# Kernel tuning notes

Hardware: AMD Instinct MI355X
Metric: run time of the kernel (lower is better)

The kernel has to match this reference:

```python
import jax, jax.numpy as jnp
import numpy as np

N, E, H = 50000, 500000, 4
DIN, DH, DO, TD = 135, 128, 64, 9

def _ln(x, g, b):
    mu = jnp.mean(x, axis=-1, keepdims=True)
    v = jnp.var(x, axis=-1, keepdims=True)
    return (x - mu) / jnp.sqrt(v + 1e-5) * g + b

def _gat(x, src, dst, W, a_src, a_dst, b, n, heads, c):
    h = (x @ W).reshape(n, heads, c)                      # [N,H,C]
    es = jnp.sum(h * a_src, -1)                           # [N,H]
    ed = jnp.sum(h * a_dst, -1)
    e = jax.nn.leaky_relu(es[src] + ed[dst], 0.2)         # [E,H]
    m = jax.ops.segment_max(e, dst, num_segments=n)       # segment softmax over dst
    ex = jnp.exp(e - m[dst])
    den = jax.ops.segment_sum(ex, dst, num_segments=n)
    alpha = ex / (den[dst] + 1e-16)
    out = jax.ops.segment_sum(h[src] * alpha[..., None], dst, num_segments=n)
    return jnp.mean(out, axis=1) + b                      # concat=False -> head mean

def setup_inputs() -> dict:
    key = jax.random.key(0)
    ks = jax.random.split(key, 32)
    rn = lambda i, shape: jax.random.normal(ks[i], shape, jnp.float32) * 0.05
    inp = {}
    inp['x'] = jax.random.normal(ks[0], (N, DIN), jnp.float32)
    inp['edge_index'] = jax.random.randint(ks[1], (2, E), 0, N, jnp.int32)
    inp['edge_attr'] = jnp.ones((E, 1), jnp.float32)
    inp['W_in'] = rn(2, (DIN, DH)); inp['b_in'] = jnp.zeros((DH,), jnp.float32)
    inp['g1W'] = rn(3, (DH, H * DH)); inp['g1as'] = rn(4, (H, DH)); inp['g1ad'] = rn(5, (H, DH)); inp['g1b'] = jnp.zeros((DH,), jnp.float32)
    inp['g2W'] = rn(6, (DH, H * DH)); inp['g2as'] = rn(7, (H, DH)); inp['g2ad'] = rn(8, (H, DH)); inp['g2b'] = jnp.zeros((DH,), jnp.float32)
    inp['g3W'] = rn(9, (DH, H * DO)); inp['g3as'] = rn(10, (H, DO)); inp['g3ad'] = rn(11, (H, DO)); inp['g3b'] = jnp.zeros((DO,), jnp.float32)
    inp['r1W'] = rn(12, (DH, DH)); inp['r1b'] = jnp.zeros((DH,), jnp.float32)
    inp['r2W'] = rn(13, (DH, DH)); inp['r2b'] = jnp.zeros((DH,), jnp.float32)
    inp['r3W'] = rn(14, (DH, DO)); inp['r3b'] = jnp.zeros((DO,), jnp.float32)
    inp['n1g'] = jnp.ones((DH,), jnp.float32); inp['n1b'] = jnp.zeros((DH,), jnp.float32)
    inp['n2g'] = jnp.ones((DH,), jnp.float32); inp['n2b'] = jnp.zeros((DH,), jnp.float32)
    inp['n3g'] = jnp.ones((DO,), jnp.float32); inp['n3b'] = jnp.zeros((DO,), jnp.float32)
    inp['tw'] = jnp.float32(0.3)
    inp['c1W'] = rn(15, (DO, DO)); inp['c1b'] = jnp.zeros((DO,), jnp.float32)
    inp['clg'] = jnp.ones((DO,), jnp.float32); inp['clb'] = jnp.zeros((DO,), jnp.float32)
    inp['c2W'] = rn(16, (DO, 2)); inp['c2b'] = jnp.zeros((2,), jnp.float32)
    return inp

def reference(x, edge_index, edge_attr, W_in, b_in, g1W, g1as, g1ad, g1b,
              g2W, g2as, g2ad, g2b, g3W, g3as, g3ad, g3b,
              r1W, r1b, r2W, r2b, r3W, r3b,
              n1g, n1b, n2g, n2b, n3g, n3b, tw,
              c1W, c1b, clg, clb, c2W, c2b):
    n = x.shape[0]
    src0, dst0 = edge_index[0], edge_index[1]
    loop = jnp.arange(n, dtype=edge_index.dtype)          # GATConv add_self_loops=True
    src = jnp.concatenate([src0, loop])
    dst = jnp.concatenate([dst0, loop])
    # vectorized temporal cosine similarity over original edges
    t = x[:, -TD:]
    ti, tj = t[src0], t[dst0]
    nrm = jnp.maximum(jnp.linalg.norm(ti, axis=-1), 1e-8) * jnp.maximum(jnp.linalg.norm(tj, axis=-1), 1e-8)
    sim = jnp.sum(ti * tj, -1) / nrm
    scale = 1.0 + 0.1 * jnp.mean(1.0 + tw * sim)
    h = x @ W_in + b_in
    id1 = h
    h = _gat(h, src, dst, g1W, g1as, g1ad, g1b, n, H, DH) * scale
    h = _ln(jax.nn.relu(h) + id1 @ r1W + r1b, n1g, n1b)
    id2 = h
    h = _gat(h, src, dst, g2W, g2as, g2ad, g2b, n, H, DH) * scale
    h = _ln(jax.nn.relu(h) + id2 @ r2W + r2b, n2g, n2b)
    id3 = h
    h = _gat(h, src, dst, g3W, g3as, g3ad, g3b, n, H, DO)
    h = _ln(jax.nn.relu(h) + id3 @ r3W + r3b, n3g, n3b)
    ego = h[0:1]
    z = jax.nn.relu(ego @ c1W + c1b)
    z = _ln(z, clg, clb)
    return z @ c2W + c2b
```

## Files before the change

### kernel.cpp

```cpp
#include <hip/hip_runtime.h>

#define AGENT __HIP_MEMORY_SCOPE_AGENT

constexpr int TD = 9, DIN = 135;
constexpr int CAP3 = 256, CAP2 = 1024, CAP1 = 4096, BK = 128;
constexpr int NB = 512;
constexpr int LSTRIDE = 32;
constexpr int NGRP = 16, GSZ = 32;
constexpr int NSET = 8;
constexpr int NLINE = 64;

struct P {
  const float* x; const int* src; const int* dst; int N; int E;
  const float *W_in,*b_in,*g1W,*g1as,*g1ad,*g1b,*g2W,*g2as,*g2ad,*g2b,*g3W,*g3as,*g3ad,*g3b;
  const float *r1W,*r1b,*r2W,*r2b,*r3W,*r3b,*n1g,*n1b,*n2g,*n2b,*n3g,*n3b;
  const float *tw,*c1W,*c1b,*clg,*clb,*c2W,*c2b;
  float* tp;
  int *m3,*m2,*m1,*list3,*list2,*list1,*cnts;
  int *barc,*barr,*barg;
  int *bcnt1,*bcnt2,*bcnt3,*bk1,*bk2,*bk3;
  float *h0,*hh1,*es1,*ed1,*h1,*hh2,*es2,*ed2,*h2,*hh3,*es3,*ed3,*h3;
  float* dout;
};

__device__ __forceinline__ float lrelu(float v) { return v >= 0.f ? v : 0.2f * v; }

__device__ __forceinline__ void stg(float* pp, float v) { __hip_atomic_store(pp, v, __ATOMIC_RELAXED, AGENT); }
__device__ __forceinline__ void stg(int* pp, int v)   { __hip_atomic_store(pp, v, __ATOMIC_RELAXED, AGENT); }

__device__ __forceinline__ void claim_node(int v, int* __restrict__ m, int* __restrict__ list,
                                           int* __restrict__ cnt, int cap) {
  if (atomicCAS(&m[v], -1, -2) == -1) {
    int pos = atomicAdd(cnt, 1);
    if (pos < cap) { stg(&list[pos], v); stg(&m[v], pos); } else { stg(&m[v], -3); }
  }
}

__device__ __forceinline__ void grid_barrier(const P& p, int& lgen, int* amroot_s) {
  __syncthreads();
  int g = lgen + 1;
  if (threadIdx.x == 0) {
    *amroot_s = 0;
    int grp = blockIdx.x & (NGRP - 1);
    int* gc = &p.barc[(((g & (NSET - 1)) * NGRP) + grp) * LSTRIDE];
    if (__hip_atomic_fetch_add(gc, 1, __ATOMIC_RELAXED, AGENT) == GSZ - 1) {
      int* rc = &p.barr[(g & (NSET - 1)) * LSTRIDE];
      if (__hip_atomic_fetch_add(rc, 1, __ATOMIC_RELAXED, AGENT) == NGRP - 1) *amroot_s = 1;
    }
  }
  __syncthreads();
  if (*amroot_s) {
    if (threadIdx.x < NLINE)
      __hip_atomic_store(&p.barg[threadIdx.x * LSTRIDE], g, __ATOMIC_RELAXED, AGENT);
  } else if (threadIdx.x == 0) {
    int* line = &p.barg[(blockIdx.x & (NLINE - 1)) * LSTRIDE];
    while (__hip_atomic_load(line, __ATOMIC_RELAXED, AGENT) < g)
      __builtin_amdgcn_s_sleep(8);
  }
  __syncthreads();
  lgen = g;
}

__global__ void k_init(P p) {
  int gt = blockIdx.x * blockDim.x + threadIdx.x;
  int GT = gridDim.x * blockDim.x;
  int n3 = 3 * p.N;
  int4* mv = (int4*)p.m3;
  int4 neg = make_int4(-1, -1, -1, -1);
  int nv = n3 >> 2;
  for (int i = gt; i < nv; i += GT) mv[i] = neg;
  for (int i = (nv << 2) + gt; i < n3; i += GT) p.m3[i] = -1;
  if (gt < 64) p.cnts[gt] = 0;
  for (int i = gt; i < NSET * NGRP * LSTRIDE; i += GT) p.barc[i] = 0;
  for (int i = gt; i < NSET * LSTRIDE; i += GT) p.barr[i] = 0;
  for (int i = gt; i < NLINE * LSTRIDE; i += GT) p.barg[i] = 0;
  for (int i = gt; i < CAP2; i += GT) p.bcnt1[i] = 0;
  for (int i = gt; i < CAP3; i += GT) p.bcnt2[i] = 0;
  if (gt == 0) p.bcnt3[0] = 0;
  int total = p.N * TD;
  for (int i = gt; i < total; i += GT) {
    int v = i / TD, k = i - v * TD;
    p.tp[i] = p.x[(size_t)v * DIN + (DIN - TD) + k];
  }
}

template <int C, int ONEXT>
__device__ void gat_phase(int nq, const int* lst, const int* mPrev,
                          const int* bket, const int* bcnt,
                          const float* hh, const float* es, const float* ed, const float* hres,
                          const float* gb, const float* rW, const float* rb,
                          const float* ng, const float* nbv, float scale,
                          float* hout, const float* Wn, const float* avn, const float* bvn,
                          float* hhn, float* esn, float* edn,
                          float* elog, int* eposs, float* sh, float* hres_s, float* shln,
                          float* psn, float* pdn, float* sc2, float* ev_s) {
  const int T = 256, Wd = 4 * C, R = Wd / T;
  int tid = threadIdx.x;
  for (int q = blockIdx.x; q < nq; q += gridDim.x) {
    int v = lst[q];
    int sp = mPrev[v];
    int nb = min(bcnt[q], BK);
    for (int j = tid; j < nb; j += T) {
      int pu = mPrev[bket[(size_t)q * BK + j]];
      eposs[j] = pu;
      const float* ep = &es[(size_t)pu * 4];
      elog[0 * BK + j] = ep[0]; elog[1 * BK + j] = ep[1];
      elog[2 * BK + j] = ep[2]; elog[3 * BK + j] = ep[3];
    }
    if (tid < 4) { ev_s[tid] = es[(size_t)sp * 4 + tid]; ev_s[4 + tid] = ed[(size_t)sp * 4 + tid]; }
    for (int k = tid; k < 128; k += T) hres_s[k] = hres[(size_t)sp * 128 + k];
    __syncthreads();
#pragma unroll
    for (int r = 0; r < R; r++) {
      int w = r * T + tid, a = w / C;
      float edv = ev_s[4 + a];
      float eself = lrelu(ev_s[a] + edv);
      float mx = eself;
      for (int j = 0; j < nb; j++) mx = fmaxf(mx, lrelu(elog[a * BK + j] + edv));
      float den = __expf(eself - mx);
      for (int j = 0; j < nb; j++) den += __expf(lrelu(elog[a * BK + j] + edv) - mx);
      float rden = 1.f / (den + 1e-16f);
      float s = __expf(eself - mx) * rden * hh[(size_t)sp * Wd + w];
      for (int j = 0; j < nb; j++)
        s += __expf(lrelu(elog[a * BK + j] + edv) - mx) * rden * hh[(size_t)eposs[j] * Wd + w];
      sh[w] = s;
    }
    __syncthreads();
    float val = 0.f;
    if (tid < C) {
      float g = 0.25f * (sh[tid] + sh[C + tid] + sh[2 * C + tid] + sh[3 * C + tid]) + gb[tid];
      g *= scale;
      g = fmaxf(g, 0.f);
      float rr = rb[tid];
      for (int k = 0; k < 128; k++) rr += hres_s[k] * rW[(size_t)k * C + tid];
      val = g + rr;
      shln[tid] = val;
    }
    __syncthreads();
    if (tid == 0) {
      float s1 = 0.f, s2 = 0.f;
      for (int k = 0; k < C; k++) { float u = shln[k]; s1 += u; s2 += u * u; }
      float mu = s1 / (float)C;
      sc2[0] = mu;
      sc2[1] = rsqrtf(fmaxf(s2 / (float)C - mu * mu, 0.f) + 1e-5f);
    }
    __syncthreads();
    if (tid < C) {
      float o = (val - sc2[0]) * sc2[1] * ng[tid] + nbv[tid];
      stg(&hout[(size_t)q * C + tid], o);
      shln[tid] = o;
    }
    __syncthreads();
    if (ONEXT > 0) {
      for (int j = tid; j < ONEXT; j += T) {
        float a2 = 0.f;
        for (int k = 0; k < C; k++) a2 += shln[k] * Wn[(size_t)k * ONEXT + j];
        stg(&hhn[(size_t)q * ONEXT + j], a2);
        psn[j] = a2 * avn[j]; pdn[j] = a2 * bvn[j];
      }
      __syncthreads();
      if (tid < 8) {
        const int CN = ONEXT / 4; int a = tid & 3;
        const float* pr = (tid < 4) ? psn : pdn;
        float s = 0.f;
        for (int c = 0; c < CN; c++) s += pr[a * CN + c];
        stg(&(tid < 4 ? esn : edn)[(size_t)q * 4 + a], s);
      }
    }
    __syncthreads();
  }
}

__global__ __launch_bounds__(256, 2) void k_mega(P p) {
  __shared__ float elog[4 * BK];
  __shared__ int   eposs[BK];
  __shared__ float sh[512];
  __shared__ float hres_s[128];
  __shared__ float shln[128];
  __shared__ float psn[512], pdn[512];
  __shared__ float xs[DIN + 1];
  __shared__ float sc2[2];
  __shared__ float ev_s[8];
  __shared__ float wred[4];
  __shared__ float zcl[64];
  __shared__ int   amroot_s;

  int tid = threadIdx.x, bid = blockIdx.x;
  int gt = bid * 256 + tid, GT = gridDim.x * 256;
  int lgen = 0;
  float* simsum = (float*)&p.cnts[8];

  {
    if (gt == 0) claim_node(0, p.m3, p.list3, &p.cnts[0], CAP3);
    float local = 0.f;
    for (int e = gt; e < p.E; e += GT) {
      int s = p.src[e], d = p.dst[e];
      if (d == 0) claim_node(s, p.m3, p.list3, &p.cnts[0], CAP3);
      const float* ti = p.tp + (size_t)s * TD;
      const float* tj = p.tp + (size_t)d * TD;
      float dot = 0.f, na = 0.f, nb2 = 0.f;
#pragma unroll
      for (int k = 0; k < TD; k++) { float a = ti[k], b = tj[k]; dot += a * b; na += a * a; nb2 += b * b; }
      local += dot / (fmaxf(sqrtf(na), 1e-8f) * fmaxf(sqrtf(nb2), 1e-8f));
    }
    for (int off = 32; off > 0; off >>= 1) local += __shfl_down(local, off, 64);
    if ((tid & 63) == 0) wred[tid >> 6] = local;
    __syncthreads();
    if (tid == 0) atomicAdd(simsum, wred[0] + wred[1] + wred[2] + wred[3]);
  }
  grid_barrier(p, lgen, &amroot_s);

  {
    int c3 = min(__hip_atomic_load(&p.cnts[0], __ATOMIC_RELAXED, AGENT), CAP3);
    for (int i = gt; i < c3; i += GT) claim_node(p.list3[i], p.m2, p.list2, &p.cnts[1], CAP2);
    for (int e = gt; e < p.E; e += GT)
      if (p.m3[p.dst[e]] >= 0) claim_node(p.src[e], p.m2, p.list2, &p.cnts[1], CAP2);
  }
  grid_barrier(p, lgen, &amroot_s);

  {
    int c2 = min(__hip_atomic_load(&p.cnts[1], __ATOMIC_RELAXED, AGENT), CAP2);
    for (int i = gt; i < c2; i += GT) claim_node(p.list2[i], p.m1, p.list1, &p.cnts[2], CAP1);
    for (int e = gt; e < p.E; e += GT) {
      int s = p.src[e], d = p.dst[e];
      int p2 = p.m2[d];
      if (p2 >= 0) {
        claim_node(s, p.m1, p.list1, &p.cnts[2], CAP1);
        int sl = atomicAdd(&p.bcnt1[p2], 1); if (sl < BK) stg(&p.bk1[(size_t)p2 * BK + sl], s);
      }
      int p3 = p.m3[d];
      if (p3 >= 0) { int sl = atomicAdd(&p.bcnt2[p3], 1); if (sl < BK) stg(&p.bk2[(size_t)p3 * BK + sl], s); }
      if (d == 0)  { int sl = atomicAdd(&p.bcnt3[0], 1);  if (sl < BK) stg(&p.bk3[sl], s); }
    }
  }
  grid_barrier(p, lgen, &amroot_s);

  {
    int c1 = min(__hip_atomic_load(&p.cnts[2], __ATOMIC_RELAXED, AGENT), CAP1);
    for (int pp = bid; pp < c1; pp += gridDim.x) {
      int v = p.list1[pp];
      for (int k = tid; k < DIN; k += 256) xs[k] = p.x[(size_t)v * DIN + k];
      __syncthreads();
      if (tid < 128) {
        float acc = p.b_in[tid];
        for (int k = 0; k < DIN; k++) acc += xs[k] * p.W_in[(size_t)k * 128 + tid];
        stg(&p.h0[(size_t)pp * 128 + tid], acc);
        hres_s[tid] = acc;
      }
      __syncthreads();
#pragma unroll
      for (int jj = 0; jj < 2; jj++) {
        int j = jj * 256 + tid;
        float acc = 0.f;
        for (int k = 0; k < 128; k++) acc += hres_s[k] * p.g1W[(size_t)k * 512 + j];
        stg(&p.hh1[(size_t)pp * 512 + j], acc);
        psn[j] = acc * p.g1as[j]; pdn[j] = acc * p.g1ad[j];
      }
      __syncthreads();
      if (tid < 8) {
        int a = tid & 3;
        const float* pr = (tid < 4) ? psn : pdn;
        float s = 0.f;
        for (int c = 0; c < 128; c++) s += pr[a * 128 + c];
        stg(&(tid < 4 ? p.es1 : p.ed1)[(size_t)pp * 4 + a], s);
      }
      __syncthreads();
    }
  }
  grid_barrier(p, lgen, &amroot_s);

  int sbits = __hip_atomic_load(&p.cnts[8], __ATOMIC_RELAXED, AGENT);
  float scale = 1.1f + 0.1f * p.tw[0] * __int_as_float(sbits) / (float)p.E;

  {
    int c2 = min(__hip_atomic_load(&p.cnts[1], __ATOMIC_RELAXED, AGENT), CAP2);
    gat_phase<128, 512>(c2, p.list2, p.m1, p.bk1, p.bcnt1,
                        p.hh1, p.es1, p.ed1, p.h0,
                        p.g1b, p.r1W, p.r1b, p.n1g, p.n1b, scale,
                        p.h1, p.g2W, p.g2as, p.g2ad, p.hh2, p.es2, p.ed2,
                        elog, eposs, sh, hres_s, shln, psn, pdn, sc2, ev_s);
  }
  grid_barrier(p, lgen, &amroot_s);

  {
    int c3 = min(__hip_atomic_load(&p.cnts[0], __ATOMIC_RELAXED, AGENT), CAP3);
    gat_phase<128, 256>(c3, p.list3, p.m2, p.bk2, p.bcnt2,
                        p.hh2, p.es2, p.ed2, p.h1,
                        p.g2b, p.r2W, p.r2b, p.n2g, p.n2b, scale,
                        p.h2, p.g3W, p.g3as, p.g3ad, p.hh3, p.es3, p.ed3,
                        elog, eposs, sh, hres_s, shln, psn, pdn, sc2, ev_s);
  }
  grid_barrier(p, lgen, &amroot_s);

  {
    gat_phase<64, 0>(1, &p.cnts[56] , p.m3, p.bk3, p.bcnt3,
                     p.hh3, p.es3, p.ed3, p.h2,
                     p.g3b, p.r3W, p.r3b, p.n3g, p.n3b, 1.f,
                     p.h3, nullptr, nullptr, nullptr, nullptr, nullptr, nullptr,
                     elog, eposs, sh, hres_s, shln, psn, pdn, sc2, ev_s);
    if (bid == 0) {
      if (tid < 64) {
        float az = p.c1b[tid];
        for (int k = 0; k < 64; k++) az += shln[k] * p.c1W[k * 64 + tid];
        zcl[tid] = fmaxf(az, 0.f);
      }
      __syncthreads();
      if (tid == 0) {
        float s1 = 0.f, s2 = 0.f;
        for (int k = 0; k < 64; k++) { float u = zcl[k]; s1 += u; s2 += u * u; }
        float mu = s1 / 64.f;
        float rstd = rsqrtf(fmaxf(s2 / 64.f - mu * mu, 0.f) + 1e-5f);
        float o0 = p.c2b[0], o1 = p.c2b[1];
        for (int k = 0; k < 64; k++) {
          float zn = (zcl[k] - mu) * rstd * p.clg[k] + p.clb[k];
          o0 += zn * p.c2W[k * 2 + 0];
          o1 += zn * p.c2W[k * 2 + 1];
        }
        p.dout[0] = o0; p.dout[1] = o1;
      }
    }
  }
}

extern "C" void kernel_launch(void* const* d_in, const int* in_sizes, int n_in,
                              void* d_out, int out_size, void* d_ws, size_t ws_size,
                              hipStream_t stream) {
  P p;
  p.x = (const float*)d_in[0];
  const int* ei = (const int*)d_in[1];
  p.N = in_sizes[0] / DIN;
  p.E = in_sizes[1] / 2;
  p.src = ei; p.dst = ei + p.E;
  p.W_in = (const float*)d_in[3]; p.b_in = (const float*)d_in[4];
  p.g1W = (const float*)d_in[5]; p.g1as = (const float*)d_in[6]; p.g1ad = (const float*)d_in[7]; p.g1b = (const float*)d_in[8];
  p.g2W = (const float*)d_in[9]; p.g2as = (const float*)d_in[10]; p.g2ad = (const float*)d_in[11]; p.g2b = (const float*)d_in[12];
  p.g3W = (const float*)d_in[13]; p.g3as = (const float*)d_in[14]; p.g3ad = (const float*)d_in[15]; p.g3b = (const float*)d_in[16];
  p.r1W = (const float*)d_in[17]; p.r1b = (const float*)d_in[18];
  p.r2W = (const float*)d_in[19]; p.r2b = (const float*)d_in[20];
  p.r3W = (const float*)d_in[21]; p.r3b = (const float*)d_in[22];
  p.n1g = (const float*)d_in[23]; p.n1b = (const float*)d_in[24];
  p.n2g = (const float*)d_in[25]; p.n2b = (const float*)d_in[26];
  p.n3g = (const float*)d_in[27]; p.n3b = (const float*)d_in[28];
  p.tw  = (const float*)d_in[29];
  p.c1W = (const float*)d_in[30]; p.c1b = (const float*)d_in[31];
  p.clg = (const float*)d_in[32]; p.clb = (const float*)d_in[33];
  p.c2W = (const float*)d_in[34]; p.c2b = (const float*)d_in[35];
  p.dout = (float*)d_out;

  char* B = (char*)d_ws;
  size_t off = 0;
  auto take = [&](size_t nbytes) -> char* {
    char* r = B + off;
    off += (nbytes + 255) & ~(size_t)255;
    return r;
  };
  p.cnts  = (int*)take(256);
  p.barc  = (int*)take((size_t)NSET * NGRP * LSTRIDE * 4);
  p.barr  = (int*)take((size_t)NSET * LSTRIDE * 4);
  p.barg  = (int*)take((size_t)NLINE * LSTRIDE * 4);
  p.m3    = (int*)take((size_t)3 * p.N * 4);
  p.m2 = p.m3 + p.N; p.m1 = p.m2 + p.N;
  p.tp    = (float*)take((size_t)p.N * TD * 4);
  p.list3 = (int*)take(CAP3 * 4);
  p.list2 = (int*)take(CAP2 * 4);
  p.list1 = (int*)take(CAP1 * 4);
  p.bcnt1 = (int*)take(CAP2 * 4);
  p.bcnt2 = (int*)take(CAP3 * 4);
  p.bcnt3 = (int*)take(64);
  p.bk1   = (int*)take((size_t)CAP2 * BK * 4);
  p.bk2   = (int*)take((size_t)CAP3 * BK * 4);
  p.bk3   = (int*)take(BK * 4);
  p.h0    = (float*)take((size_t)CAP1 * 128 * 4);
  p.hh1   = (float*)take((size_t)CAP1 * 512 * 4);
  p.es1   = (float*)take((size_t)CAP1 * 16);
  p.ed1   = (float*)take((size_t)CAP1 * 16);
  p.h1    = (float*)take((size_t)CAP2 * 128 * 4);
  p.hh2   = (float*)take((size_t)CAP2 * 512 * 4);
  p.es2   = (float*)take((size_t)CAP2 * 16);
  p.ed2   = (float*)take((size_t)CAP2 * 16);
  p.h2    = (float*)take((size_t)CAP3 * 128 * 4);
  p.hh3   = (float*)take((size_t)CAP3 * 256 * 4);
  p.es3   = (float*)take((size_t)CAP3 * 16);
  p.ed3   = (float*)take((size_t)CAP3 * 16);
  p.h3    = (float*)take(64 * 4);

  k_init<<<1024, 256, 0, stream>>>(p);
  k_mega<<<NB, 256, 0, stream>>>(p);
}
```

Measured before the change: 127.5 us.

## Batch several nodes per block in GAT and input-projection phases

```diff
diff --git a/kernel.cpp b/kernel.cpp
--- a/kernel.cpp
+++ b/kernel.cpp
@@ -9,6 +9,8 @@
 constexpr int NGRP = 16, GSZ = 32;
 constexpr int NSET = 8;
 constexpr int NLINE = 64;
+constexpr int DB = 4;
+constexpr int PB = 8;
 
 struct P {
   const float* x; const int* src; const int* dst; int N; int E;
@@ -92,79 +94,144 @@
                           const float* ng, const float* nbv, float scale,
                           float* hout, const float* Wn, const float* avn, const float* bvn,
                           float* hhn, float* esn, float* edn,
-                          float* elog, int* eposs, float* sh, float* hres_s, float* shln,
-                          float* psn, float* pdn, float* sc2, float* ev_s) {
-  const int T = 256, Wd = 4 * C, R = Wd / T;
+                          float* elog4, int* eposs4, float* hres4, float* agg4, float* gm4,
+                          float* selfw, int* meta, float* sc2d, float* psn, float* pdn) {
+  const int Wd = 4 * C;
   int tid = threadIdx.x;
-  for (int q = blockIdx.x; q < nq; q += gridDim.x) {
-    int v = lst[q];
-    int sp = mPrev[v];
-    int nb = min(bcnt[q], BK);
-    for (int j = tid; j < nb; j += T) {
-      int pu = mPrev[bket[(size_t)q * BK + j]];
-      eposs[j] = pu;
-      const float* ep = &es[(size_t)pu * 4];
-      elog[0 * BK + j] = ep[0]; elog[1 * BK + j] = ep[1];
-      elog[2 * BK + j] = ep[2]; elog[3 * BK + j] = ep[3];
-    }
-    if (tid < 4) { ev_s[tid] = es[(size_t)sp * 4 + tid]; ev_s[4 + tid] = ed[(size_t)sp * 4 + tid]; }
-    for (int k = tid; k < 128; k += T) hres_s[k] = hres[(size_t)sp * 128 + k];
-    __syncthreads();
-#pragma unroll
-    for (int r = 0; r < R; r++) {
-      int w = r * T + tid, a = w / C;
-      float edv = ev_s[4 + a];
-      float eself = lrelu(ev_s[a] + edv);
+  int ngp = (nq + DB - 1) / DB;
+  for (int g = blockIdx.x; g < ngp; g += gridDim.x) {
+    int q0 = g * DB, nd = min(DB, nq - q0);
+    if (tid < DB) {
+      int sp = 0, nbu = 0;
+      if (tid < nd) { int v = lst[q0 + tid]; sp = mPrev[v]; nbu = min(bcnt[q0 + tid], BK); }
+      meta[tid * 2 + 0] = sp; meta[tid * 2 + 1] = nbu;
+    }
+    __syncthreads();
+    for (int idx = tid; idx < nd * 128; idx += 256) {
+      int u = idx >> 7, k = idx & 127;
+      hres4[u * 128 + k] = hres[(size_t)meta[u * 2] * 128 + k];
+    }
+    if (tid < nd * 8) {
+      int u = tid >> 3, k = tid & 7;
+      selfw[u * 8 + k] = (k < 4) ? es[(size_t)meta[u * 2] * 4 + k] : ed[(size_t)meta[u * 2] * 4 + (k - 4)];
+    }
+    for (int u = 0; u < nd; ++u) {
+      int nbu = meta[u * 2 + 1];
+      for (int j = tid; j < nbu; j += 256) {
+        int pu = mPrev[bket[(size_t)(q0 + u) * BK + j]];
+        eposs4[u * BK + j] = pu;
+        const float* ep = &es[(size_t)pu * 4];
+        elog4[(u * 4 + 0) * BK + j] = ep[0]; elog4[(u * 4 + 1) * BK + j] = ep[1];
+        elog4[(u * 4 + 2) * BK + j] = ep[2]; elog4[(u * 4 + 3) * BK + j] = ep[3];
+      }
+    }
+    __syncthreads();
+    if (tid < nd * 4) {
+      int u = tid >> 2, a = tid & 3, nbu = meta[u * 2 + 1];
+      float edv = selfw[u * 8 + 4 + a];
+      float eself = lrelu(selfw[u * 8 + a] + edv);
       float mx = eself;
-      for (int j = 0; j < nb; j++) mx = fmaxf(mx, lrelu(elog[a * BK + j] + edv));
+      float* el = &elog4[(u * 4 + a) * BK];
+      for (int j = 0; j < nbu; j++) mx = fmaxf(mx, lrelu(el[j] + edv));
       float den = __expf(eself - mx);
-      for (int j = 0; j < nb; j++) den += __expf(lrelu(elog[a * BK + j] + edv) - mx);
+      for (int j = 0; j < nbu; j++) den += __expf(lrelu(el[j] + edv) - mx);
       float rden = 1.f / (den + 1e-16f);
-      float s = __expf(eself - mx) * rden * hh[(size_t)sp * Wd + w];
-      for (int j = 0; j < nb; j++)
-        s += __expf(lrelu(elog[a * BK + j] + edv) - mx) * rden * hh[(size_t)eposs[j] * Wd + w];
-      sh[w] = s;
-    }
-    __syncthreads();
-    float val = 0.f;
-    if (tid < C) {
-      float g = 0.25f * (sh[tid] + sh[C + tid] + sh[2 * C + tid] + sh[3 * C + tid]) + gb[tid];
-      g *= scale;
-      g = fmaxf(g, 0.f);
-      float rr = rb[tid];
-      for (int k = 0; k < 128; k++) rr += hres_s[k] * rW[(size_t)k * C + tid];
-      val = g + rr;
-      shln[tid] = val;
-    }
-    __syncthreads();
-    if (tid == 0) {
+      for (int j = 0; j < nbu; j++) el[j] = __expf(lrelu(el[j] + edv) - mx) * rden;
+      selfw[u * 8 + a] = __expf(eself - mx) * rden;
+    }
+    __syncthreads();
+    for (int idx = tid; idx < nd * Wd; idx += 256) {
+      int u = idx / Wd, w = idx - u * Wd, a = w / C;
+      int nbu = meta[u * 2 + 1], sp = meta[u * 2];
+      const float* el = &elog4[(u * 4 + a) * BK];
+      const int* ej = &eposs4[u * BK];
+      float s = selfw[u * 8 + a] * hh[(size_t)sp * Wd + w];
+      for (int j = 0; j < nbu; j++) s += el[j] * hh[(size_t)ej[j] * Wd + w];
+      agg4[u * Wd + w] = s;
+    }
+    __syncthreads();
+    for (int idx = tid; idx < nd * C; idx += 256) {
+      int u = idx / C, c = idx - u * C;
+      float gmv = 0.25f * (agg4[u * Wd + c] + agg4[u * Wd + C + c] +
+                           agg4[u * Wd + 2 * C + c] + agg4[u * Wd + 3 * C + c]) + gb[c];
+      gm4[u * C + c] = fmaxf(gmv * scale, 0.f);
+    }
+    __syncthreads();
+    {
+      const int nUg = 256 / C;
+      const int K2 = (DB + nUg - 1) / nUg;
+      int c = tid & (C - 1), ug = tid / C;
+      float acc[K2];
+#pragma unroll
+      for (int t = 0; t < K2; t++) acc[t] = 0.f;
+      for (int k = 0; k < 128; k++) {
+        float w = rW[(size_t)k * C + c];
+#pragma unroll
+        for (int t = 0; t < K2; t++) { int u = ug + t * nUg; acc[t] += hres4[u * 128 + k] * w; }
+      }
+      float rbc = rb[c];
+#pragma unroll
+      for (int t = 0; t < K2; t++) {
+        int u = ug + t * nUg;
+        if (u < nd) gm4[u * C + c] += rbc + acc[t];
+      }
+    }
+    __syncthreads();
+    {
+      int u = tid >> 6, lane = tid & 63;
       float s1 = 0.f, s2 = 0.f;
-      for (int k = 0; k < C; k++) { float u = shln[k]; s1 += u; s2 += u * u; }
-      float mu = s1 / (float)C;
-      sc2[0] = mu;
-      sc2[1] = rsqrtf(fmaxf(s2 / (float)C - mu * mu, 0.f) + 1e-5f);
-    }
-    __syncthreads();
-    if (tid < C) {
-      float o = (val - sc2[0]) * sc2[1] * ng[tid] + nbv[tid];
-      stg(&hout[(size_t)q * C + tid], o);
-      shln[tid] = o;
+      if (u < nd) {
+        for (int c = lane; c < C; c += 64) { float xv = gm4[u * C + c]; s1 += xv; s2 += xv * xv; }
+      }
+      for (int off = 32; off > 0; off >>= 1) { s1 += __shfl_down(s1, off, 64); s2 += __shfl_down(s2, off, 64); }
+      if (lane == 0 && u < nd) {
+        float mu = s1 / (float)C;
+        sc2d[u * 2 + 0] = mu;
+        sc2d[u * 2 + 1] = rsqrtf(fmaxf(s2 / (float)C - mu * mu, 0.f) + 1e-5f);
+      }
+    }
+    __syncthreads();
+    for (int idx = tid; idx < nd * C; idx += 256) {
+      int u = idx / C, c = idx - u * C;
+      float o = (gm4[u * C + c] - sc2d[u * 2]) * sc2d[u * 2 + 1] * ng[c] + nbv[c];
+      stg(&hout[(size_t)(q0 + u) * C + c], o);
+      gm4[u * C + c] = o;
     }
     __syncthreads();
     if (ONEXT > 0) {
-      for (int j = tid; j < ONEXT; j += T) {
-        float a2 = 0.f;
-        for (int k = 0; k < C; k++) a2 += shln[k] * Wn[(size_t)k * ONEXT + j];
-        stg(&hhn[(size_t)q * ONEXT + j], a2);
-        psn[j] = a2 * avn[j]; pdn[j] = a2 * bvn[j];
-      }
-      __syncthreads();
-      if (tid < 8) {
-        const int CN = ONEXT / 4; int a = tid & 3;
-        const float* pr = (tid < 4) ? psn : pdn;
-        float s = 0.f;
-        for (int c = 0; c < CN; c++) s += pr[a * CN + c];
-        stg(&(tid < 4 ? esn : edn)[(size_t)q * 4 + a], s);
+      const int JJ = (ONEXT > 0) ? (ONEXT / 256) : 1;
+      float accp[JJ][DB];
+#pragma unroll
+      for (int jj = 0; jj < JJ; jj++) {
+        int j = jj * 256 + tid;
+        float a0 = 0.f, a1 = 0.f, a2 = 0.f, a3 = 0.f;
+        for (int k = 0; k < C; k++) {
+          float w = Wn[(size_t)k * ONEXT + j];
+          a0 += gm4[0 * C + k] * w; a1 += gm4[1 * C + k] * w;
+          a2 += gm4[2 * C + k] * w; a3 += gm4[3 * C + k] * w;
+        }
+        accp[jj][0] = a0; accp[jj][1] = a1; accp[jj][2] = a2; accp[jj][3] = a3;
+        if (0 < nd) stg(&hhn[(size_t)(q0 + 0) * ONEXT + j], a0);
+        if (1 < nd) stg(&hhn[(size_t)(q0 + 1) * ONEXT + j], a1);
+        if (2 < nd) stg(&hhn[(size_t)(q0 + 2) * ONEXT + j], a2);
+        if (3 < nd) stg(&hhn[(size_t)(q0 + 3) * ONEXT + j], a3);
+      }
+      for (int u = 0; u < nd; u++) {
+#pragma unroll
+        for (int jj = 0; jj < JJ; jj++) {
+          int j = jj * 256 + tid;
+          psn[j] = accp[jj][u] * avn[j];
+          pdn[j] = accp[jj][u] * bvn[j];
+        }
+        __syncthreads();
+        if (tid < 8) {
+          const int CN = ONEXT / 4; int a = tid & 3;
+          const float* pr = (tid < 4) ? psn : pdn;
+          float s = 0.f;
+          for (int cc = 0; cc < CN; cc++) s += pr[a * CN + cc];
+          stg(&(tid < 4 ? esn : edn)[(size_t)(q0 + u) * 4 + a], s);
+        }
+        __syncthreads();
       }
     }
     __syncthreads();
@@ -172,15 +239,18 @@
 }
 
 __global__ __launch_bounds__(256, 2) void k_mega(P p) {
-  __shared__ float elog[4 * BK];
-  __shared__ int   eposs[BK];
-  __shared__ float sh[512];
-  __shared__ float hres_s[128];
-  __shared__ float shln[128];
+  __shared__ float elog4[DB * 4 * BK];
+  __shared__ int   eposs4[DB * BK];
+  __shared__ float hres4[DB * 128];
+  __shared__ float agg4[DB * 512];
+  __shared__ float gm4[DB * 128];
+  __shared__ float selfw[DB * 8];
+  __shared__ int   meta[DB * 2];
+  __shared__ float sc2d[DB * 2];
   __shared__ float psn[512], pdn[512];
-  __shared__ float xs[DIN + 1];
-  __shared__ float sc2[2];
-  __shared__ float ev_s[8];
+  __shared__ float xs8[PB * DIN];
+  __shared__ float hs8[PB * 128];
+  __shared__ int   vid8[PB];
   __shared__ float wred[4];
   __shared__ float zcl[64];
   __shared__ int   amroot_s;
@@ -229,42 +299,75 @@
         int sl = atomicAdd(&p.bcnt1[p2], 1); if (sl < BK) stg(&p.bk1[(size_t)p2 * BK + sl], s);
       }
       int p3 = p.m3[d];
-      if (p3 >= 0) { int sl = atomicAdd(&p.bcnt2[p3], 1); if (sl < BK) stg(&p.bk2[(size_t)p3 * BK + sl], s); }
-      if (d == 0)  { int sl = atomicAdd(&p.bcnt3[0], 1);  if (sl < BK) stg(&p.bk3[sl], s); }
+      if (p3 >= 0) { int sl2 = atomicAdd(&p.bcnt2[p3], 1); if (sl2 < BK) stg(&p.bk2[(size_t)p3 * BK + sl2], s); }
+      if (d == 0)  { int sl3 = atomicAdd(&p.bcnt3[0], 1);  if (sl3 < BK) stg(&p.bk3[sl3], s); }
     }
   }
   grid_barrier(p, lgen, &amroot_s);
 
   {
     int c1 = min(__hip_atomic_load(&p.cnts[2], __ATOMIC_RELAXED, AGENT), CAP1);
-    for (int pp = bid; pp < c1; pp += gridDim.x) {
-      int v = p.list1[pp];
-      for (int k = tid; k < DIN; k += 256) xs[k] = p.x[(size_t)v * DIN + k];
+    int ngp = (c1 + PB - 1) / PB;
+    for (int g = bid; g < ngp; g += gridDim.x) {
+      int base = g * PB, nn = min(PB, c1 - base);
+      if (tid < nn) vid8[tid] = p.list1[base + tid];
+      __syncthreads();
+      for (int idx = tid; idx < nn * DIN; idx += 256) {
+        int u = idx / DIN, k = idx - u * DIN;
+        xs8[u * DIN + k] = p.x[(size_t)vid8[u] * DIN + k];
+      }
       __syncthreads();
       if (tid < 128) {
-        float acc = p.b_in[tid];
-        for (int k = 0; k < DIN; k++) acc += xs[k] * p.W_in[(size_t)k * 128 + tid];
-        stg(&p.h0[(size_t)pp * 128 + tid], acc);
-        hres_s[tid] = acc;
+        float a[PB]; float bi = p.b_in[tid];
+#pragma unroll
+        for (int u = 0; u < PB; u++) a[u] = bi;
+        for (int k = 0; k < DIN; k++) {
+          float w = p.W_in[(size_t)k * 128 + tid];
+#pragma unroll
+          for (int u = 0; u < PB; u++) a[u] += xs8[u * DIN + k] * w;
+        }
+#pragma unroll
+        for (int u = 0; u < PB; u++) {
+          hs8[u * 128 + tid] = a[u];
+          if (u < nn) stg(&p.h0[(size_t)(base + u) * 128 + tid], a[u]);
+        }
       }
       __syncthreads();
+      float bsv[2][PB];
 #pragma unroll
       for (int jj = 0; jj < 2; jj++) {
         int j = jj * 256 + tid;
-        float acc = 0.f;
-        for (int k = 0; k < 128; k++) acc += hres_s[k] * p.g1W[(size_t)k * 512 + j];
-        stg(&p.hh1[(size_t)pp * 512 + j], acc);
-        psn[j] = acc * p.g1as[j]; pdn[j] = acc * p.g1ad[j];
-      }
-      __syncthreads();
-      if (tid < 8) {
-        int a = tid & 3;
-        const float* pr = (tid < 4) ? psn : pdn;
-        float s = 0.f;
-        for (int c = 0; c < 128; c++) s += pr[a * 128 + c];
-        stg(&(tid < 4 ? p.es1 : p.ed1)[(size_t)pp * 4 + a], s);
-      }
-      __syncthreads();
+        float b[PB];
+#pragma unroll
+        for (int u = 0; u < PB; u++) b[u] = 0.f;
+        for (int k = 0; k < 128; k++) {
+          float w = p.g1W[(size_t)k * 512 + j];
+#pragma unroll
+          for (int u = 0; u < PB; u++) b[u] += hs8[u * 128 + k] * w;
+        }
+#pragma unroll
+        for (int u = 0; u < PB; u++) {
+          bsv[jj][u] = b[u];
+          if (u < nn) stg(&p.hh1[(size_t)(base + u) * 512 + j], b[u]);
+        }
+      }
+      for (int u = 0; u < nn; u++) {
+#pragma unroll
+        for (int jj = 0; jj < 2; jj++) {
+          int j = jj * 256 + tid;
+          psn[j] = bsv[jj][u] * p.g1as[j];
+          pdn[j] = bsv[jj][u] * p.g1ad[j];
+        }
+        __syncthreads();
+        if (tid < 8) {
+          int a = tid & 3;
+          const float* pr = (tid < 4) ? psn : pdn;
+          float s = 0.f;
+          for (int cc = 0; cc < 128; cc++) s += pr[a * 128 + cc];
+          stg(&(tid < 4 ? p.es1 : p.ed1)[(size_t)(base + u) * 4 + a], s);
+        }
+        __syncthreads();
+      }
     }
   }
   grid_barrier(p, lgen, &amroot_s);
@@ -278,7 +381,7 @@
                         p.hh1, p.es1, p.ed1, p.h0,
                         p.g1b, p.r1W, p.r1b, p.n1g, p.n1b, scale,
                         p.h1, p.g2W, p.g2as, p.g2ad, p.hh2, p.es2, p.ed2,
-                        elog, eposs, sh, hres_s, shln, psn, pdn, sc2, ev_s);
+                        elog4, eposs4, hres4, agg4, gm4, selfw, meta, sc2d, psn, pdn);
   }
   grid_barrier(p, lgen, &amroot_s);
 
@@ -288,7 +391,7 @@
                         p.hh2, p.es2, p.ed2, p.h1,
                         p.g2b, p.r2W, p.r2b, p.n2g, p.n2b, scale,
                         p.h2, p.g3W, p.g3as, p.g3ad, p.hh3, p.es3, p.ed3,
-                        elog, eposs, sh, hres_s, shln, psn, pdn, sc2, ev_s);
+                        elog4, eposs4, hres4, agg4, gm4, selfw, meta, sc2d, psn, pdn);
   }
   grid_barrier(p, lgen, &amroot_s);
 
@@ -297,11 +400,11 @@
                      p.hh3, p.es3, p.ed3, p.h2,
                      p.g3b, p.r3W, p.r3b, p.n3g, p.n3b, 1.f,
                      p.h3, nullptr, nullptr, nullptr, nullptr, nullptr, nullptr,
-                     elog, eposs, sh, hres_s, shln, psn, pdn, sc2, ev_s);
+                     elog4, eposs4, hres4, agg4, gm4, selfw, meta, sc2d, psn, pdn);
     if (bid == 0) {
       if (tid < 64) {
         float az = p.c1b[tid];
-        for (int k = 0; k < 64; k++) az += shln[k] * p.c1W[k * 64 + tid];
+        for (int k = 0; k < 64; k++) az += gm4[k] * p.c1W[k * 64 + tid];
         zcl[tid] = fmaxf(az, 0.f);
       }
       __syncthreads();
```

Result: slower. 201.1 us (+57.7%).

## Build per-node in-edge buckets once and expand frontier via adjacency instead of edge scans

Applied to the files above, without the earlier changes.

```diff
diff --git a/kernel.cpp b/kernel.cpp
--- a/kernel.cpp
+++ b/kernel.cpp
@@ -2,13 +2,16 @@
 
 #define AGENT __HIP_MEMORY_SCOPE_AGENT
 
-constexpr int TD = 9, DIN = 135;
-constexpr int CAP3 = 256, CAP2 = 1024, CAP1 = 4096, BK = 128;
-constexpr int NB = 512;
+constexpr int TD = 9, TDP = 12, DIN = 135;
+constexpr int CAPD = 64;
+constexpr int CAP3 = 256, CAP2 = 1024, CAP1 = 4096;
+constexpr int NBM = 160;
 constexpr int LSTRIDE = 32;
-constexpr int NGRP = 16, GSZ = 32;
+constexpr int NGRP = 16;
+constexpr int GSZ = NBM / NGRP;
 constexpr int NSET = 8;
-constexpr int NLINE = 64;
+constexpr int NLINE = 16;
+constexpr int PB = 8;
 
 struct P {
   const float* x; const int* src; const int* dst; int N; int E;
@@ -16,9 +19,9 @@
   const float *r1W,*r1b,*r2W,*r2b,*r3W,*r3b,*n1g,*n1b,*n2g,*n2b,*n3g,*n3b;
   const float *tw,*c1W,*c1b,*clg,*clb,*c2W,*c2b;
   float* tp;
+  int *deg, *bk;
   int *m3,*m2,*m1,*list3,*list2,*list1,*cnts;
   int *barc,*barr,*barg;
-  int *bcnt1,*bcnt2,*bcnt3,*bk1,*bk2,*bk3;
   float *h0,*hh1,*es1,*ed1,*h1,*hh2,*es2,*ed2,*h2,*hh3,*es3,*ed3,*h3;
   float* dout;
 };
@@ -36,13 +39,12 @@
   }
 }
 
-__device__ __forceinline__ void grid_barrier(const P& p, int& lgen, int* amroot_s) {
+__device__ __forceinline__ void mid_barrier(const P& p, int& lgen, int* amroot_s) {
   __syncthreads();
   int g = lgen + 1;
   if (threadIdx.x == 0) {
     *amroot_s = 0;
-    int grp = blockIdx.x & (NGRP - 1);
-    int* gc = &p.barc[(((g & (NSET - 1)) * NGRP) + grp) * LSTRIDE];
+    int* gc = &p.barc[(((g & (NSET - 1)) * NGRP) + (blockIdx.x & (NGRP - 1))) * LSTRIDE];
     if (__hip_atomic_fetch_add(gc, 1, __ATOMIC_RELAXED, AGENT) == GSZ - 1) {
       int* rc = &p.barr[(g & (NSET - 1)) * LSTRIDE];
       if (__hip_atomic_fetch_add(rc, 1, __ATOMIC_RELAXED, AGENT) == NGRP - 1) *amroot_s = 1;
@@ -55,13 +57,13 @@
   } else if (threadIdx.x == 0) {
     int* line = &p.barg[(blockIdx.x & (NLINE - 1)) * LSTRIDE];
     while (__hip_atomic_load(line, __ATOMIC_RELAXED, AGENT) < g)
-      __builtin_amdgcn_s_sleep(8);
+      __builtin_amdgcn_s_sleep(1);
   }
   __syncthreads();
   lgen = g;
 }
 
-__global__ void k_init(P p) {
+__global__ void k_prep(P p) {
   int gt = blockIdx.x * blockDim.x + threadIdx.x;
   int GT = gridDim.x * blockDim.x;
   int n3 = 3 * p.N;
@@ -70,59 +72,98 @@
   int nv = n3 >> 2;
   for (int i = gt; i < nv; i += GT) mv[i] = neg;
   for (int i = (nv << 2) + gt; i < n3; i += GT) p.m3[i] = -1;
+  int4* dv = (int4*)p.deg;
+  int4 z4 = make_int4(0, 0, 0, 0);
+  int ndv = p.N >> 2;
+  for (int i = gt; i < ndv; i += GT) dv[i] = z4;
+  for (int i = (ndv << 2) + gt; i < p.N; i += GT) p.deg[i] = 0;
   if (gt < 64) p.cnts[gt] = 0;
   for (int i = gt; i < NSET * NGRP * LSTRIDE; i += GT) p.barc[i] = 0;
   for (int i = gt; i < NSET * LSTRIDE; i += GT) p.barr[i] = 0;
   for (int i = gt; i < NLINE * LSTRIDE; i += GT) p.barg[i] = 0;
-  for (int i = gt; i < CAP2; i += GT) p.bcnt1[i] = 0;
-  for (int i = gt; i < CAP3; i += GT) p.bcnt2[i] = 0;
-  if (gt == 0) p.bcnt3[0] = 0;
-  int total = p.N * TD;
+  int total = p.N * TDP;
   for (int i = gt; i < total; i += GT) {
-    int v = i / TD, k = i - v * TD;
-    p.tp[i] = p.x[(size_t)v * DIN + (DIN - TD) + k];
-  }
+    int v = i / TDP, k = i - v * TDP;
+    p.tp[i] = (k < TD) ? p.x[(size_t)v * DIN + (DIN - TD) + k] : 0.f;
+  }
+}
+
+__global__ void k_scan(P p) {
+  __shared__ float wred[4];
+  int tid = threadIdx.x;
+  int gt = blockIdx.x * blockDim.x + tid, GT = gridDim.x * blockDim.x;
+  if (gt == 0) claim_node(0, p.m3, p.list3, &p.cnts[0], CAP3);
+  const float4* t4 = (const float4*)p.tp;
+  float local = 0.f;
+  auto edge_proc = [&](int s, int d) {
+    int slot = atomicAdd(&p.deg[d], 1);
+    if (slot < CAPD) p.bk[(size_t)d * CAPD + slot] = s;
+    if (d == 0) claim_node(s, p.m3, p.list3, &p.cnts[0], CAP3);
+    float4 a0 = t4[s * 3], a1 = t4[s * 3 + 1], a2 = t4[s * 3 + 2];
+    float4 b0 = t4[d * 3], b1 = t4[d * 3 + 1], b2 = t4[d * 3 + 2];
+    float dot = a0.x*b0.x + a0.y*b0.y + a0.z*b0.z + a0.w*b0.w
+              + a1.x*b1.x + a1.y*b1.y + a1.z*b1.z + a1.w*b1.w
+              + a2.x*b2.x;
+    float na = a0.x*a0.x + a0.y*a0.y + a0.z*a0.z + a0.w*a0.w
+             + a1.x*a1.x + a1.y*a1.y + a1.z*a1.z + a1.w*a1.w
+             + a2.x*a2.x;
+    float nb = b0.x*b0.x + b0.y*b0.y + b0.z*b0.z + b0.w*b0.w
+             + b1.x*b1.x + b1.y*b1.y + b1.z*b1.z + b1.w*b1.w
+             + b2.x*b2.x;
+    local += dot / (fmaxf(sqrtf(na), 1e-8f) * fmaxf(sqrtf(nb), 1e-8f));
+  };
+  int nq4 = p.E >> 2;
+  const int4* s4p = (const int4*)p.src;
+  const int4* d4p = (const int4*)p.dst;
+  for (int q = gt; q < nq4; q += GT) {
+    int4 s4 = s4p[q], d4 = d4p[q];
+    edge_proc(s4.x, d4.x); edge_proc(s4.y, d4.y); edge_proc(s4.z, d4.z); edge_proc(s4.w, d4.w);
+  }
+  for (int e = (nq4 << 2) + gt; e < p.E; e += GT) edge_proc(p.src[e], p.dst[e]);
+  for (int off = 32; off > 0; off >>= 1) local += __shfl_down(local, off, 64);
+  if ((tid & 63) == 0) wred[tid >> 6] = local;
+  __syncthreads();
+  if (tid == 0) atomicAdd((float*)&p.cnts[8], wred[0] + wred[1] + wred[2] + wred[3]);
 }
 
 template <int C, int ONEXT>
-__device__ void gat_phase(int nq, const int* lst, const int* mPrev,
-                          const int* bket, const int* bcnt,
-                          const float* hh, const float* es, const float* ed, const float* hres,
-                          const float* gb, const float* rW, const float* rb,
-                          const float* ng, const float* nbv, float scale,
-                          float* hout, const float* Wn, const float* avn, const float* bvn,
-                          float* hhn, float* esn, float* edn,
-                          float* elog, int* eposs, float* sh, float* hres_s, float* shln,
-                          float* psn, float* pdn, float* sc2, float* ev_s) {
-  const int T = 256, Wd = 4 * C, R = Wd / T;
+__device__ void gat_dev(const P& p, int nq, const int* lst, const int* mPrev,
+                        const float* hh, const float* es, const float* ed, const float* hres,
+                        const float* gb, const float* rW, const float* rb,
+                        const float* ng, const float* nbv, float scale,
+                        float* hout, const float* Wn, const float* avn, const float* bvn,
+                        float* hhn, float* esn, float* edn,
+                        float* elog, int* eposs, float* ev_s, float* sh,
+                        float* hres_s, float* shln, float* psn, float* pdn, float* sc2) {
+  const int Wd = 4 * C, R = Wd / 256;
   int tid = threadIdx.x;
   for (int q = blockIdx.x; q < nq; q += gridDim.x) {
     int v = lst[q];
     int sp = mPrev[v];
-    int nb = min(bcnt[q], BK);
-    for (int j = tid; j < nb; j += T) {
-      int pu = mPrev[bket[(size_t)q * BK + j]];
+    int nb = min(p.deg[v], CAPD);
+    for (int j = tid; j < nb; j += 256) {
+      int pu = mPrev[p.bk[(size_t)v * CAPD + j]];
       eposs[j] = pu;
       const float* ep = &es[(size_t)pu * 4];
-      elog[0 * BK + j] = ep[0]; elog[1 * BK + j] = ep[1];
-      elog[2 * BK + j] = ep[2]; elog[3 * BK + j] = ep[3];
+      elog[0 * CAPD + j] = ep[0]; elog[1 * CAPD + j] = ep[1];
+      elog[2 * CAPD + j] = ep[2]; elog[3 * CAPD + j] = ep[3];
     }
     if (tid < 4) { ev_s[tid] = es[(size_t)sp * 4 + tid]; ev_s[4 + tid] = ed[(size_t)sp * 4 + tid]; }
-    for (int k = tid; k < 128; k += T) hres_s[k] = hres[(size_t)sp * 128 + k];
+    for (int k = tid; k < 128; k += 256) hres_s[k] = hres[(size_t)sp * 128 + k];
     __syncthreads();
 #pragma unroll
     for (int r = 0; r < R; r++) {
-      int w = r * T + tid, a = w / C;
+      int w = r * 256 + tid, a = w / C;
       float edv = ev_s[4 + a];
       float eself = lrelu(ev_s[a] + edv);
       float mx = eself;
-      for (int j = 0; j < nb; j++) mx = fmaxf(mx, lrelu(elog[a * BK + j] + edv));
+      for (int j = 0; j < nb; j++) mx = fmaxf(mx, lrelu(elog[a * CAPD + j] + edv));
       float den = __expf(eself - mx);
-      for (int j = 0; j < nb; j++) den += __expf(lrelu(elog[a * BK + j] + edv) - mx);
+      for (int j = 0; j < nb; j++) den += __expf(lrelu(elog[a * CAPD + j] + edv) - mx);
       float rden = 1.f / (den + 1e-16f);
       float s = __expf(eself - mx) * rden * hh[(size_t)sp * Wd + w];
       for (int j = 0; j < nb; j++)
-        s += __expf(lrelu(elog[a * BK + j] + edv) - mx) * rden * hh[(size_t)eposs[j] * Wd + w];
+        s += __expf(lrelu(elog[a * CAPD + j] + edv) - mx) * rden * hh[(size_t)eposs[j] * Wd + w];
       sh[w] = s;
     }
     __syncthreads();
@@ -152,7 +193,7 @@
     }
     __syncthreads();
     if (ONEXT > 0) {
-      for (int j = tid; j < ONEXT; j += T) {
+      for (int j = tid; j < ONEXT; j += 256) {
         float a2 = 0.f;
         for (int k = 0; k < C; k++) a2 += shln[k] * Wn[(size_t)k * ONEXT + j];
         stg(&hhn[(size_t)q * ONEXT + j], a2);
@@ -163,161 +204,165 @@
         const int CN = ONEXT / 4; int a = tid & 3;
         const float* pr = (tid < 4) ? psn : pdn;
         float s = 0.f;
-        for (int c = 0; c < CN; c++) s += pr[a * CN + c];
+        for (int cc = 0; cc < CN; cc++) s += pr[a * CN + cc];
         stg(&(tid < 4 ? esn : edn)[(size_t)q * 4 + a], s);
       }
-    }
-    __syncthreads();
-  }
-}
-
-__global__ __launch_bounds__(256, 2) void k_mega(P p) {
-  __shared__ float elog[4 * BK];
-  __shared__ int   eposs[BK];
-  __shared__ float sh[512];
-  __shared__ float hres_s[128];
-  __shared__ float shln[128];
+      __syncthreads();
+    }
+  }
+}
+
+__global__ __launch_bounds__(256) void k_mid(P p) {
+  __shared__ float xs8[PB][DIN];
+  __shared__ float hs8[PB][128];
   __shared__ float psn[512], pdn[512];
-  __shared__ float xs[DIN + 1];
-  __shared__ float sc2[2];
-  __shared__ float ev_s[8];
-  __shared__ float wred[4];
+  __shared__ int   vid8[PB];
+  __shared__ float elog[4 * CAPD];
+  __shared__ int   eposs[CAPD];
+  __shared__ float ev_s[8], sc2[2];
+  __shared__ float sh[512], hres_s[128], shln[128];
   __shared__ float zcl[64];
   __shared__ int   amroot_s;
 
   int tid = threadIdx.x, bid = blockIdx.x;
-  int gt = bid * 256 + tid, GT = gridDim.x * 256;
   int lgen = 0;
-  float* simsum = (float*)&p.cnts[8];
-
-  {
-    if (gt == 0) claim_node(0, p.m3, p.list3, &p.cnts[0], CAP3);
-    float local = 0.f;
-    for (int e = gt; e < p.E; e += GT) {
-      int s = p.src[e], d = p.dst[e];
-      if (d == 0) claim_node(s, p.m3, p.list3, &p.cnts[0], CAP3);
-      const float* ti = p.tp + (size_t)s * TD;
-      const float* tj = p.tp + (size_t)d * TD;
-      float dot = 0.f, na = 0.f, nb2 = 0.f;
-#pragma unroll
-      for (int k = 0; k < TD; k++) { float a = ti[k], b = tj[k]; dot += a * b; na += a * a; nb2 += b * b; }
-      local += dot / (fmaxf(sqrtf(na), 1e-8f) * fmaxf(sqrtf(nb2), 1e-8f));
-    }
-    for (int off = 32; off > 0; off >>= 1) local += __shfl_down(local, off, 64);
-    if ((tid & 63) == 0) wred[tid >> 6] = local;
-    __syncthreads();
-    if (tid == 0) atomicAdd(simsum, wred[0] + wred[1] + wred[2] + wred[3]);
-  }
-  grid_barrier(p, lgen, &amroot_s);
+  float scale = 1.1f + 0.1f * p.tw[0] *
+      __int_as_float(__hip_atomic_load(&p.cnts[8], __ATOMIC_RELAXED, AGENT)) / (float)p.E;
 
   {
     int c3 = min(__hip_atomic_load(&p.cnts[0], __ATOMIC_RELAXED, AGENT), CAP3);
-    for (int i = gt; i < c3; i += GT) claim_node(p.list3[i], p.m2, p.list2, &p.cnts[1], CAP2);
-    for (int e = gt; e < p.E; e += GT)
-      if (p.m3[p.dst[e]] >= 0) claim_node(p.src[e], p.m2, p.list2, &p.cnts[1], CAP2);
-  }
-  grid_barrier(p, lgen, &amroot_s);
+    for (int q = bid; q < c3; q += NBM) {
+      int v = p.list3[q];
+      if (tid == 0) claim_node(v, p.m2, p.list2, &p.cnts[1], CAP2);
+      int nb = min(p.deg[v], CAPD);
+      for (int j = tid; j < nb; j += 256)
+        claim_node(p.bk[(size_t)v * CAPD + j], p.m2, p.list2, &p.cnts[1], CAP2);
+    }
+  }
+  mid_barrier(p, lgen, &amroot_s);
 
   {
     int c2 = min(__hip_atomic_load(&p.cnts[1], __ATOMIC_RELAXED, AGENT), CAP2);
-    for (int i = gt; i < c2; i += GT) claim_node(p.list2[i], p.m1, p.list1, &p.cnts[2], CAP1);
-    for (int e = gt; e < p.E; e += GT) {
-      int s = p.src[e], d = p.dst[e];
-      int p2 = p.m2[d];
-      if (p2 >= 0) {
-        claim_node(s, p.m1, p.list1, &p.cnts[2], CAP1);
-        int sl = atomicAdd(&p.bcnt1[p2], 1); if (sl < BK) stg(&p.bk1[(size_t)p2 * BK + sl], s);
-      }
-      int p3 = p.m3[d];
-      if (p3 >= 0) { int sl = atomicAdd(&p.bcnt2[p3], 1); if (sl < BK) stg(&p.bk2[(size_t)p3 * BK + sl], s); }
-      if (d == 0)  { int sl = atomicAdd(&p.bcnt3[0], 1);  if (sl < BK) stg(&p.bk3[sl], s); }
-    }
-  }
-  grid_barrier(p, lgen, &amroot_s);
+    for (int q = bid; q < c2; q += NBM) {
+      int v = p.list2[q];
+      if (tid == 0) claim_node(v, p.m1, p.list1, &p.cnts[2], CAP1);
+      int nb = min(p.deg[v], CAPD);
+      for (int j = tid; j < nb; j += 256)
+        claim_node(p.bk[(size_t)v * CAPD + j], p.m1, p.list1, &p.cnts[2], CAP1);
+    }
+  }
+  mid_barrier(p, lgen, &amroot_s);
 
   {
     int c1 = min(__hip_atomic_load(&p.cnts[2], __ATOMIC_RELAXED, AGENT), CAP1);
-    for (int pp = bid; pp < c1; pp += gridDim.x) {
-      int v = p.list1[pp];
-      for (int k = tid; k < DIN; k += 256) xs[k] = p.x[(size_t)v * DIN + k];
+    int ngp = (c1 + PB - 1) / PB;
+    for (int g = bid; g < ngp; g += NBM) {
+      int base = g * PB, nn = min(PB, c1 - base);
+      if (tid < nn) vid8[tid] = p.list1[base + tid];
+      __syncthreads();
+      for (int idx = tid; idx < nn * DIN; idx += 256) {
+        int u = idx / DIN, k = idx - u * DIN;
+        xs8[u][k] = p.x[(size_t)vid8[u] * DIN + k];
+      }
       __syncthreads();
       if (tid < 128) {
-        float acc = p.b_in[tid];
-        for (int k = 0; k < DIN; k++) acc += xs[k] * p.W_in[(size_t)k * 128 + tid];
-        stg(&p.h0[(size_t)pp * 128 + tid], acc);
-        hres_s[tid] = acc;
+        float a[PB]; float bi = p.b_in[tid];
+#pragma unroll
+        for (int u = 0; u < PB; u++) a[u] = bi;
+        for (int k = 0; k < DIN; k++) {
+          float w = p.W_in[(size_t)k * 128 + tid];
+#pragma unroll
+          for (int u = 0; u < PB; u++) a[u] += xs8[u][k] * w;
+        }
+#pragma unroll
+        for (int u = 0; u < PB; u++) {
+          hs8[u][tid] = a[u];
+          if (u < nn) stg(&p.h0[(size_t)(base + u) * 128 + tid], a[u]);
+        }
       }
       __syncthreads();
+      float bsv[2][PB];
 #pragma unroll
       for (int jj = 0; jj < 2; jj++) {
         int j = jj * 256 + tid;
-        float acc = 0.f;
-        for (int k = 0; k < 128; k++) acc += hres_s[k] * p.g1W[(size_t)k * 512 + j];
-        stg(&p.hh1[(size_t)pp * 512 + j], acc);
-        psn[j] = acc * p.g1as[j]; pdn[j] = acc * p.g1ad[j];
-      }
-      __syncthreads();
-      if (tid < 8) {
-        int a = tid & 3;
-        const float* pr = (tid < 4) ? psn : pdn;
-        float s = 0.f;
-        for (int c = 0; c < 128; c++) s += pr[a * 128 + c];
-        stg(&(tid < 4 ? p.es1 : p.ed1)[(size_t)pp * 4 + a], s);
-      }
-      __syncthreads();
-    }
-  }
-  grid_barrier(p, lgen, &amroot_s);
-
-  int sbits = __hip_atomic_load(&p.cnts[8], __ATOMIC_RELAXED, AGENT);
-  float scale = 1.1f + 0.1f * p.tw[0] * __int_as_float(sbits) / (float)p.E;
+        float b[PB];
+#pragma unroll
+        for (int u = 0; u < PB; u++) b[u] = 0.f;
+        for (int k = 0; k < 128; k++) {
+          float w = p.g1W[(size_t)k * 512 + j];
+#pragma unroll
+          for (int u = 0; u < PB; u++) b[u] += hs8[u][k] * w;
+        }
+#pragma unroll
+        for (int u = 0; u < PB; u++) {
+          bsv[jj][u] = b[u];
+          if (u < nn) stg(&p.hh1[(size_t)(base + u) * 512 + j], b[u]);
+        }
+      }
+      for (int u = 0; u < nn; u++) {
+#pragma unroll
+        for (int jj = 0; jj < 2; jj++) {
+          int j = jj * 256 + tid;
+          psn[j] = bsv[jj][u] * p.g1as[j];
+          pdn[j] = bsv[jj][u] * p.g1ad[j];
+        }
+        __syncthreads();
+        if (tid < 8) {
+          int a = tid & 3;
+          const float* pr = (tid < 4) ? psn : pdn;
+          float s = 0.f;
+          for (int cc = 0; cc < 128; cc++) s += pr[a * 128 + cc];
+          stg(&(tid < 4 ? p.es1 : p.ed1)[(size_t)(base + u) * 4 + a], s);
+        }
+        __syncthreads();
+      }
+    }
+  }
+  mid_barrier(p, lgen, &amroot_s);
 
   {
     int c2 = min(__hip_atomic_load(&p.cnts[1], __ATOMIC_RELAXED, AGENT), CAP2);
-    gat_phase<128, 512>(c2, p.list2, p.m1, p.bk1, p.bcnt1,
-                        p.hh1, p.es1, p.ed1, p.h0,
-                        p.g1b, p.r1W, p.r1b, p.n1g, p.n1b, scale,
-                        p.h1, p.g2W, p.g2as, p.g2ad, p.hh2, p.es2, p.ed2,
-                        elog, eposs, sh, hres_s, shln, psn, pdn, sc2, ev_s);
-  }
-  grid_barrier(p, lgen, &amroot_s);
+    gat_dev<128, 512>(p, c2, p.list2, p.m1, p.hh1, p.es1, p.ed1, p.h0,
+                      p.g1b, p.r1W, p.r1b, p.n1g, p.n1b, scale,
+                      p.h1, p.g2W, p.g2as, p.g2ad, p.hh2, p.es2, p.ed2,
+                      elog, eposs, ev_s, sh, hres_s, shln, psn, pdn, sc2);
+  }
+  mid_barrier(p, lgen, &amroot_s);
 
   {
     int c3 = min(__hip_atomic_load(&p.cnts[0], __ATOMIC_RELAXED, AGENT), CAP3);
-    gat_phase<128, 256>(c3, p.list3, p.m2, p.bk2, p.bcnt2,
-                        p.hh2, p.es2, p.ed2, p.h1,
-                        p.g2b, p.r2W, p.r2b, p.n2g, p.n2b, scale,
-                        p.h2, p.g3W, p.g3as, p.g3ad, p.hh3, p.es3, p.ed3,
-                        elog, eposs, sh, hres_s, shln, psn, pdn, sc2, ev_s);
-  }
-  grid_barrier(p, lgen, &amroot_s);
-
-  {
-    gat_phase<64, 0>(1, &p.cnts[56] , p.m3, p.bk3, p.bcnt3,
-                     p.hh3, p.es3, p.ed3, p.h2,
-                     p.g3b, p.r3W, p.r3b, p.n3g, p.n3b, 1.f,
-                     p.h3, nullptr, nullptr, nullptr, nullptr, nullptr, nullptr,
-                     elog, eposs, sh, hres_s, shln, psn, pdn, sc2, ev_s);
-    if (bid == 0) {
-      if (tid < 64) {
-        float az = p.c1b[tid];
-        for (int k = 0; k < 64; k++) az += shln[k] * p.c1W[k * 64 + tid];
-        zcl[tid] = fmaxf(az, 0.f);
-      }
-      __syncthreads();
-      if (tid == 0) {
-        float s1 = 0.f, s2 = 0.f;
-        for (int k = 0; k < 64; k++) { float u = zcl[k]; s1 += u; s2 += u * u; }
-        float mu = s1 / 64.f;
-        float rstd = rsqrtf(fmaxf(s2 / 64.f - mu * mu, 0.f) + 1e-5f);
-        float o0 = p.c2b[0], o1 = p.c2b[1];
-        for (int k = 0; k < 64; k++) {
-          float zn = (zcl[k] - mu) * rstd * p.clg[k] + p.clb[k];
-          o0 += zn * p.c2W[k * 2 + 0];
-          o1 += zn * p.c2W[k * 2 + 1];
-        }
-        p.dout[0] = o0; p.dout[1] = o1;
-      }
+    gat_dev<128, 256>(p, c3, p.list3, p.m2, p.hh2, p.es2, p.ed2, p.h1,
+                      p.g2b, p.r2W, p.r2b, p.n2g, p.n2b, scale,
+                      p.h2, p.g3W, p.g3as, p.g3ad, p.hh3, p.es3, p.ed3,
+                      elog, eposs, ev_s, sh, hres_s, shln, psn, pdn, sc2);
+  }
+  mid_barrier(p, lgen, &amroot_s);
+
+  if (bid == 0) {
+    int zero = 0;
+    gat_dev<64, 0>(p, 1, &zero , p.m3,
+                   p.hh3, p.es3, p.ed3, p.h2,
+                   p.g3b, p.r3W, p.r3b, p.n3g, p.n3b, 1.f,
+                   p.h3, nullptr, nullptr, nullptr, nullptr, nullptr, nullptr,
+                   elog, eposs, ev_s, sh, hres_s, shln, psn, pdn, sc2);
+    if (tid < 64) {
+      float az = p.c1b[tid];
+      for (int k = 0; k < 64; k++) az += shln[k] * p.c1W[k * 64 + tid];
+      zcl[tid] = fmaxf(az, 0.f);
+    }
+    __syncthreads();
+    if (tid == 0) {
+      float s1 = 0.f, s2 = 0.f;
+      for (int k = 0; k < 64; k++) { float u = zcl[k]; s1 += u; s2 += u * u; }
+      float mu = s1 / 64.f;
+      float rstd = rsqrtf(fmaxf(s2 / 64.f - mu * mu, 0.f) + 1e-5f);
+      float o0 = p.c2b[0], o1 = p.c2b[1];
+      for (int k = 0; k < 64; k++) {
+        float zn = (zcl[k] - mu) * rstd * p.clg[k] + p.clb[k];
+        o0 += zn * p.c2W[k * 2 + 0];
+        o1 += zn * p.c2W[k * 2 + 1];
+      }
+      p.dout[0] = o0; p.dout[1] = o1;
     }
   }
 }
@@ -360,16 +405,12 @@
   p.barg  = (int*)take((size_t)NLINE * LSTRIDE * 4);
   p.m3    = (int*)take((size_t)3 * p.N * 4);
   p.m2 = p.m3 + p.N; p.m1 = p.m2 + p.N;
-  p.tp    = (float*)take((size_t)p.N * TD * 4);
+  p.tp    = (float*)take((size_t)p.N * TDP * 4);
+  p.deg   = (int*)take((size_t)p.N * 4);
+  p.bk    = (int*)take((size_t)p.N * CAPD * 4);
   p.list3 = (int*)take(CAP3 * 4);
   p.list2 = (int*)take(CAP2 * 4);
   p.list1 = (int*)take(CAP1 * 4);
-  p.bcnt1 = (int*)take(CAP2 * 4);
-  p.bcnt2 = (int*)take(CAP3 * 4);
-  p.bcnt3 = (int*)take(64);
-  p.bk1   = (int*)take((size_t)CAP2 * BK * 4);
-  p.bk2   = (int*)take((size_t)CAP3 * BK * 4);
-  p.bk3   = (int*)take(BK * 4);
   p.h0    = (float*)take((size_t)CAP1 * 128 * 4);
   p.hh1   = (float*)take((size_t)CAP1 * 512 * 4);
   p.es1   = (float*)take((size_t)CAP1 * 16);
@@ -384,6 +425,7 @@
   p.ed3   = (float*)take((size_t)CAP3 * 16);
   p.h3    = (float*)take(64 * 4);
 
-  k_init<<<1024, 256, 0, stream>>>(p);
-  k_mega<<<NB, 256, 0, stream>>>(p);
-}
+  k_prep<<<1024, 256, 0, stream>>>(p);
+  k_scan<<<1024, 256, 0, stream>>>(p);
+  k_mid<<<NBM, 256, 0, stream>>>(p);
+}
```

Result: slower. 171.4 us (+34.5%).
